# Kernel tuning notes

Measured on AMD Instinct MI355X. Metric: run time of the kernel, lower is better.

## Reference

```python
import jax, jax.numpy as jnp
import numpy as np

N = 50          # n_nodes
TAU = 1.0       # sinkhorn_tau
ITERS = 5       # sinkhorn_iters
ALPHA = 1.0


def _psi_fn(x, W1, b1, W2, b2):
    # x: [B, N, F]
    h = jax.nn.leaky_relu(x @ W1 + b1)          # [B, N, H], slope 0.01 matches torch default
    M = jax.nn.leaky_relu(h @ W2 + b2)          # [B, N, N]
    P = jnp.exp(M / TAU)
    for _ in range(ITERS):                      # alternating row/col normalization
        P = P / jnp.sum(P, axis=2, keepdims=True)
        P = P / jnp.sum(P, axis=1, keepdims=True)
    return P


def _hungarian(cost):
    """O(n^3) Hungarian (shortest augmenting path, like scipy.linear_sum_assignment).
    cost: [n, n] numpy. Returns col index assigned to each row (minimizes cost)."""
    n = cost.shape[0]
    INF = 1e18
    u = np.zeros(n + 1)
    v = np.zeros(n + 1)
    p = np.zeros(n + 1, dtype=np.int64)   # p[j] = row matched to column j (1-based)
    for i in range(1, n + 1):
        p[0] = i
        j0 = 0
        minv = np.full(n + 1, INF)
        way = np.zeros(n + 1, dtype=np.int64)
        used = np.zeros(n + 1, dtype=bool)
        while True:
            used[j0] = True
            i0 = p[j0]
            cur = cost[i0 - 1, :] - u[i0] - v[1:]
            free = ~used[1:]
            better = free & (cur < minv[1:])
            mv = minv[1:]
            mv[better] = cur[better]
            way[1:][better] = j0
            cand = np.where(free, mv, INF)
            j1 = int(np.argmin(cand)) + 1
            delta = cand[j1 - 1]
            u[p[used]] += delta
            v[used] -= delta
            mv[free] -= delta
            j0 = j1
            if p[j0] == 0:
                break
        while j0 != 0:
            j1 = way[j0]
            p[j0] = p[j1]
            j0 = j1
    row_to_col = np.zeros(n, dtype=np.int64)
    for j in range(1, n + 1):
        if p[j] > 0:
            row_to_col[p[j] - 1] = j - 1
    return row_to_col


def setup_inputs() -> dict:
    key = jax.random.key(0)
    k1, k2, k3, k4, k5 = jax.random.split(key, 5)
    B, F, H = 128, 1024, 4096
    s1 = 1.0 / np.sqrt(F)
    s2 = 1.0 / np.sqrt(H)
    x = jax.random.normal(k1, (B, N, F), dtype=jnp.float32)
    W1 = jax.random.uniform(k2, (F, H), minval=-s1, maxval=s1, dtype=jnp.float32)
    b1 = jax.random.uniform(k3, (H,), minval=-s1, maxval=s1, dtype=jnp.float32)
    W2 = jax.random.uniform(k4, (H, N), minval=-s2, maxval=s2, dtype=jnp.float32)
    b2 = jax.random.uniform(k5, (N,), minval=-s2, maxval=s2, dtype=jnp.float32)
    return {"x": x, "W1": W1, "b1": b1, "W2": W2, "b2": b2, "do_round": 1}


def reference(x, W1, b1, W2, b2, do_round):
    psi = _psi_fn(x, W1, b1, W2, b2)            # [B, N, N] doubly-stochastic (approx)
    if do_round:
        batch = np.asarray(psi)
        B = batch.shape[0]
        perms_np = np.zeros((B, N, N), dtype=np.float32)
        rows = np.arange(N)
        for i in range(B):
            cols = _hungarian(-batch[i])        # maximize psi == minimize -psi
            perms_np[i, rows, cols] = 1.0
        perms = jnp.asarray(perms_np)
        dist = jnp.sum(psi * perms, axis=(1, 2)) / N   # [B]
        X = (1.0 - ALPHA) * perms + ALPHA * psi
        return (psi, perms, X, dist)
    return (psi, None, None, None)
```

## Files before the change

### kernel.cpp

```cpp
#include <hip/hip_runtime.h>

#define NMAT 50
#define BATCH 128
#define FDIM 1024
#define HDIM 4096
#define ROWS 6400
#define PSIZE 320000
#define HINF 1e18

#define WS_M_OFF   0
#define WS_XH_OFF  10240000LL
#define WS_XL_OFF  23347200LL
#define WS_W1H_OFF 36454400LL
#define WS_W1L_OFF 44843008LL
#define WS_H_OFF   53231616LL
#define WS_MIN     (WS_H_OFF + 128LL * HDIM * 4)

typedef __bf16 bf16x8 __attribute__((ext_vector_type(8)));
typedef float f32x4 __attribute__((ext_vector_type(4)));
typedef double f64x4 __attribute__((ext_vector_type(4)));
typedef unsigned short u16;

__device__ __forceinline__ float bf16_to_f32(unsigned short h) {
  return __uint_as_float(((unsigned int)h) << 16);
}
__device__ __forceinline__ unsigned short f32_to_bf16(float f) {
  unsigned int u = __float_as_uint(f);
  u += 0x7FFFu + ((u >> 16) & 1u);
  return (unsigned short)(u >> 16);
}

__device__ __forceinline__ void gload16(const u16* g, u16* l) {
  __builtin_amdgcn_global_load_lds(
      (const __attribute__((address_space(1))) unsigned int*)g,
      (__attribute__((address_space(3))) unsigned int*)l, 16, 0, 0);
}

__device__ __forceinline__ double wave_min_f64(double x) {
  union { double d; int i[2]; } u, t;
  u.d = x;
#define DPP_MIN_STEP(ctrl)                                                   \
  t.i[0] = __builtin_amdgcn_update_dpp(u.i[0], u.i[0], ctrl, 0xf, 0xf, false);\
  t.i[1] = __builtin_amdgcn_update_dpp(u.i[1], u.i[1], ctrl, 0xf, 0xf, false);\
  u.d = fmin(u.d, t.d);
  DPP_MIN_STEP(0x111)
  DPP_MIN_STEP(0x112)
  DPP_MIN_STEP(0x114)
  DPP_MIN_STEP(0x118)
  DPP_MIN_STEP(0x142)
  DPP_MIN_STEP(0x143)
#undef DPP_MIN_STEP
  union { double d; int i[2]; } r;
  r.i[0] = __builtin_amdgcn_readlane(u.i[0], 63);
  r.i[1] = __builtin_amdgcn_readlane(u.i[1], 63);
  return r.d;
}

__global__ __launch_bounds__(256) void convert_x(
    const float* __restrict__ X, u16* __restrict__ Xh, u16* __restrict__ Xl) {
  int t = threadIdx.x;
  int mt = blockIdx.x >> 5, k0b = blockIdx.x & 31;
  size_t outbase = (size_t)blockIdx.x * 4096;
#pragma unroll
  for (int it = 0; it < 2; ++it) {
    int idx = t + it * 256;
    int m = idx & 127, kg = idx >> 7;
    const float* src = X + (size_t)(mt * 128 + m) * FDIM + k0b * 32 + kg * 8;
    float4 v0 = *(const float4*)src;
    float4 v1 = *(const float4*)(src + 4);
    float f[8] = {v0.x, v0.y, v0.z, v0.w, v1.x, v1.y, v1.z, v1.w};
    unsigned short h[8], l[8];
#pragma unroll
    for (int j = 0; j < 8; ++j) {
      h[j] = f32_to_bf16(f[j]);
      l[j] = f32_to_bf16(f[j] - bf16_to_f32(h[j]));
    }
    uint4 hv, lv;
    hv.x = h[0] | ((unsigned)h[1] << 16); hv.y = h[2] | ((unsigned)h[3] << 16);
    hv.z = h[4] | ((unsigned)h[5] << 16); hv.w = h[6] | ((unsigned)h[7] << 16);
    lv.x = l[0] | ((unsigned)l[1] << 16); lv.y = l[2] | ((unsigned)l[3] << 16);
    lv.z = l[4] | ((unsigned)l[5] << 16); lv.w = l[6] | ((unsigned)l[7] << 16);
    size_t off = outbase + (size_t)(kg * 128 + m) * 8;
    *(uint4*)&Xh[off] = hv;
    *(uint4*)&Xl[off] = lv;
  }
}

__global__ __launch_bounds__(256) void convert_w1(
    const float* __restrict__ W1, u16* __restrict__ Wh, u16* __restrict__ Wl) {
  int t = threadIdx.x;
  int nt = blockIdx.x >> 5, k0b = blockIdx.x & 31;
  size_t outbase = (size_t)blockIdx.x * 4096;
#pragma unroll
  for (int it = 0; it < 2; ++it) {
    int idx = t + it * 256;
    int n = idx & 127, kg = idx >> 7;
    float f[8];
#pragma unroll
    for (int j = 0; j < 8; ++j)
      f[j] = W1[(size_t)(k0b * 32 + kg * 8 + j) * HDIM + nt * 128 + n];
    unsigned short h[8], l[8];
#pragma unroll
    for (int j = 0; j < 8; ++j) {
      h[j] = f32_to_bf16(f[j]);
      l[j] = f32_to_bf16(f[j] - bf16_to_f32(h[j]));
    }
    uint4 hv, lv;
    hv.x = h[0] | ((unsigned)h[1] << 16); hv.y = h[2] | ((unsigned)h[3] << 16);
    hv.z = h[4] | ((unsigned)h[5] << 16); hv.w = h[6] | ((unsigned)h[7] << 16);
    lv.x = l[0] | ((unsigned)l[1] << 16); lv.y = l[2] | ((unsigned)l[3] << 16);
    lv.z = l[4] | ((unsigned)l[5] << 16); lv.w = l[6] | ((unsigned)l[7] << 16);
    size_t off = outbase + (size_t)(kg * 128 + n) * 8;
    *(uint4*)&Wh[off] = hv;
    *(uint4*)&Wl[off] = lv;
  }
}

__global__ __launch_bounds__(256) void gemm1_mfma(
    const u16* __restrict__ Ah_, const u16* __restrict__ Al_,
    const u16* __restrict__ Bh_, const u16* __restrict__ Bl_,
    const float* __restrict__ b1,
    float* __restrict__ Hout,
    int mt0) {
  __shared__ __align__(16) u16 Ah[4096];
  __shared__ __align__(16) u16 Al[4096];
  __shared__ __align__(16) u16 Bh[4096];
  __shared__ __align__(16) u16 Bl[4096];
  int t = threadIdx.x;
  int wave = t >> 6, lane = t & 63;
  int nt = blockIdx.x & 31;
  int mtl = blockIdx.x >> 5;
  int wm = wave >> 1, wn = wave & 1;
  int fr = lane & 15, fg = lane >> 4;

  f32x4 acc[4][4];
#pragma unroll
  for (int i = 0; i < 4; ++i)
#pragma unroll
    for (int j = 0; j < 4; ++j) acc[i][j] = (f32x4){0.f, 0.f, 0.f, 0.f};

  const u16* pAh = Ah_ + (size_t)(mt0 + mtl) * 32 * 4096;
  const u16* pAl = Al_ + (size_t)(mt0 + mtl) * 32 * 4096;
  const u16* pBh = Bh_ + (size_t)nt * 32 * 4096;
  const u16* pBl = Bl_ + (size_t)nt * 32 * 4096;
  int so = wave * 1024 + lane * 8;
  int ld = wave * 1024;

  for (int k0b = 0; k0b < 32; ++k0b) {
    __syncthreads();
    size_t sb = (size_t)k0b * 4096;
    gload16(pAh + sb + so,       &Ah[ld]);
    gload16(pAh + sb + so + 512, &Ah[ld + 512]);
    gload16(pAl + sb + so,       &Al[ld]);
    gload16(pAl + sb + so + 512, &Al[ld + 512]);
    gload16(pBh + sb + so,       &Bh[ld]);
    gload16(pBh + sb + so + 512, &Bh[ld + 512]);
    gload16(pBl + sb + so,       &Bl[ld]);
    gload16(pBl + sb + so + 512, &Bl[ld + 512]);
    __syncthreads();
    bf16x8 ah[4], al[4], bh[4], bl[4];
#pragma unroll
    for (int i = 0; i < 4; ++i) {
      int arow = (fg * 128 + wm * 64 + i * 16 + fr) * 8;
      ah[i] = *(const bf16x8*)&Ah[arow];
      al[i] = *(const bf16x8*)&Al[arow];
      int brow = (fg * 128 + wn * 64 + i * 16 + fr) * 8;
      bh[i] = *(const bf16x8*)&Bh[brow];
      bl[i] = *(const bf16x8*)&Bl[brow];
    }
#pragma unroll
    for (int i = 0; i < 4; ++i)
#pragma unroll
      for (int j = 0; j < 4; ++j)
        acc[i][j] = __builtin_amdgcn_mfma_f32_16x16x32_bf16(ah[i], bh[j], acc[i][j], 0, 0, 0);
#pragma unroll
    for (int i = 0; i < 4; ++i)
#pragma unroll
      for (int j = 0; j < 4; ++j)
        acc[i][j] = __builtin_amdgcn_mfma_f32_16x16x32_bf16(ah[i], bl[j], acc[i][j], 0, 0, 0);
#pragma unroll
    for (int i = 0; i < 4; ++i)
#pragma unroll
      for (int j = 0; j < 4; ++j)
        acc[i][j] = __builtin_amdgcn_mfma_f32_16x16x32_bf16(al[i], bh[j], acc[i][j], 0, 0, 0);
  }

  int colb = nt * 128 + wn * 64 + fr;
  int rowb = mtl * 128 + wm * 64 + fg * 4;
#pragma unroll
  for (int j = 0; j < 4; ++j) {
    float bias = b1[colb + j * 16];
#pragma unroll
    for (int i = 0; i < 4; ++i)
#pragma unroll
      for (int r = 0; r < 4; ++r) {
        float v = acc[i][j][r] + bias;
        v = v >= 0.0f ? v : 0.01f * v;
        Hout[(size_t)(rowb + i * 16 + r) * HDIM + colb + j * 16] = v;
      }
  }
}

__global__ __launch_bounds__(256) void gemm2_mfma(
    const float* __restrict__ hchunk,
    const float* __restrict__ W2,
    double* __restrict__ Mpart,
    int row0) {
  __shared__ __align__(16) float hs[64 * 68];
  __shared__ __align__(16) float w2s[64 * 68];
  int t = threadIdx.x;
  int wave = t >> 6, lane = t & 63;
  int kz = blockIdx.y;
  int fr = lane & 15, fk = lane >> 4;
  const float* hbase = hchunk + (size_t)blockIdx.x * 64 * HDIM;

  f64x4 z4 = (f64x4){0.0, 0.0, 0.0, 0.0};
  f64x4 pA = __builtin_amdgcn_mfma_f64_16x16x4f64((double)lane, 1.0, z4, 0, 0, 0);
  f64x4 pB = __builtin_amdgcn_mfma_f64_16x16x4f64(1.0, (double)lane, z4, 0, 0, 0);
  int aAlt = ((int)pA[0]) & 3;
  int bAlt = ((int)pB[0]) & 3;
  int ai = aAlt ? (lane >> 2) : fr;
  int ak = aAlt ? (lane & 3) : fk;
  int bj = bAlt ? (lane >> 2) : fr;
  int bk = bAlt ? (lane & 3) : fk;
  f64x4 p1 = __builtin_amdgcn_mfma_f64_16x16x4f64((double)ai, 1.0, z4, 0, 0, 0);
  f64x4 p2 = __builtin_amdgcn_mfma_f64_16x16x4f64(1.0, (double)bj, z4, 0, 0, 0);
  int di[4], dj[4];
#pragma unroll
  for (int r = 0; r < 4; ++r) {
    di[r] = (((int)p1[r]) >> 2) & 15;
    dj[r] = (((int)p2[r]) >> 2) & 15;
  }

  f64x4 acc[4], acc2[4];
#pragma unroll
  for (int nt = 0; nt < 4; ++nt) { acc[nt] = z4; acc2[nt] = z4; }

  int arow = (wave * 16 + ai) * 68 + ak;
  for (int k0 = kz * 1024; k0 < kz * 1024 + 1024; k0 += 64) {
    __syncthreads();
    {
      int row = t >> 2, seg = (t & 3) * 16;
      const float4* src = (const float4*)(hbase + (size_t)row * HDIM + k0 + seg);
      float4* dst = (float4*)&hs[row * 68 + seg];
      dst[0] = src[0]; dst[1] = src[1]; dst[2] = src[2]; dst[3] = src[3];
    }
    for (int idx = t; idx < 64 * 64; idx += 256) {
      int kk = idx >> 6, n = idx & 63;
      w2s[kk * 68 + n] = (n < NMAT) ? W2[(size_t)(k0 + kk) * NMAT + n] : 0.0f;
    }
    __syncthreads();
#pragma unroll
    for (int kk = 0; kk < 64; kk += 8) {
      double av0 = (double)hs[arow + kk];
      double av1 = (double)hs[arow + kk + 4];
#pragma unroll
      for (int nt = 0; nt < 4; ++nt) {
        double bv = (double)w2s[(kk + bk) * 68 + nt * 16 + bj];
        acc[nt] = __builtin_amdgcn_mfma_f64_16x16x4f64(av0, bv, acc[nt], 0, 0, 0);
      }
#pragma unroll
      for (int nt = 0; nt < 4; ++nt) {
        double bv = (double)w2s[(kk + 4 + bk) * 68 + nt * 16 + bj];
        acc2[nt] = __builtin_amdgcn_mfma_f64_16x16x4f64(av1, bv, acc2[nt], 0, 0, 0);
      }
    }
  }
  double* Mout = Mpart + (size_t)kz * PSIZE;
  int rowbase = row0 + blockIdx.x * 64 + wave * 16;
#pragma unroll
  for (int nt = 0; nt < 4; ++nt) {
    f64x4 s = acc[nt] + acc2[nt];
#pragma unroll
    for (int r = 0; r < 4; ++r) {
      int col = nt * 16 + dj[r];
      if (col < NMAT)
        Mout[(size_t)(rowbase + di[r]) * NMAT + col] = s[r];
    }
  }
}

__global__ __launch_bounds__(64) void sinkhorn_hungarian(
    const double* __restrict__ Mpart, const float* __restrict__ b2,
    float* __restrict__ out_psi, float* __restrict__ out_X,
    float* __restrict__ out_perms, float* __restrict__ out_dist) {
  int b = blockIdx.x, lane = threadIdx.x;
  __shared__ double P[2500];
  __shared__ double cost[2500];
  __shared__ double rs[50];
  __shared__ double u[51];
  __shared__ int p[51];
  __shared__ int wayl[51];
  const size_t base = (size_t)b * 2500;

  for (int e = lane; e < 2500; e += 64) {
    double m = Mpart[base + e] + Mpart[PSIZE + base + e] +
               Mpart[2 * PSIZE + base + e] + Mpart[3 * PSIZE + base + e];
    m += (double)b2[e % 50];
    m = m >= 0.0 ? m : 0.01 * m;
    P[e] = exp(m);
  }
  __syncthreads();
  for (int it = 0; it < 5; ++it) {
    if (lane < 50) { double s = 0; for (int j = 0; j < 50; ++j) s += P[lane * 50 + j]; rs[lane] = s; }
    __syncthreads();
    for (int e = lane; e < 2500; e += 64) P[e] /= rs[e / 50];
    __syncthreads();
    if (lane < 50) { double s = 0; for (int r = 0; r < 50; ++r) s += P[r * 50 + lane]; rs[lane] = s; }
    __syncthreads();
    for (int e = lane; e < 2500; e += 64) P[e] /= rs[e % 50];
    __syncthreads();
  }
  for (int e = lane; e < 2500; e += 64) {
    float f = (float)P[e];
    out_psi[base + e] = f;
    out_X[base + e] = f;
    cost[e] = -P[e];
  }
  if (lane < 51) { u[lane] = 0.0; p[lane] = 0; }
  __syncthreads();

  double v = 0.0;
  bool lactive = lane < NMAT;
  for (int i = 1; i <= NMAT; ++i) {
    bool used = false;
    int way = 0;
    int j0 = 0, j1 = 0;
    for (int guard = 0; guard < 64; ++guard) {
      if (lane == j0 - 1) used = true;
      int i0 = (j0 == 0) ? i : p[j0];
      double ui0 = u[i0];
      double cand = HINF;
      if (lactive && !used) {
        cand = cost[(i0 - 1) * NMAT + lane] - ui0 - v;
        way = j0;
      }
      double m = wave_min_f64(cand);
      unsigned long long bal = __ballot(cand == m);
      j1 = (int)__builtin_ctzll(bal) + 1;
      double delta = m;
      __syncthreads();
      if (used) { v -= delta; u[p[lane + 1]] += delta; }
      if (lane == 63) u[i] += delta;
      __syncthreads();
      j0 = j1;
      if (p[j0] == 0) break;
    }
    if (lactive) wayl[lane + 1] = way;
    __syncthreads();
    if (lane == 0) {
      int j = j1;
      for (int step = 0; step < 64 && j != 0; ++step) {
        int jw = wayl[j];
        p[j] = (jw == 0) ? i : p[jw];
        j = jw;
      }
    }
    __syncthreads();
  }

  size_t pbase = (size_t)b * 2500;
  for (int e = lane; e < 2500; e += 64) out_perms[pbase + e] = 0.0f;
  __syncthreads();
  double val = 0.0;
  if (lactive) {
    int row = p[lane + 1] - 1;
    if (row < 0) row = 0;
    if (row > 49) row = 49;
    out_perms[pbase + (size_t)row * NMAT + lane] = 1.0f;
    val = P[(size_t)row * NMAT + lane];
  }
#pragma unroll
  for (int s = 32; s > 0; s >>= 1) val += __shfl_xor(val, s, 64);
  if (lane == 0) out_dist[b] = (float)(val / (double)NMAT);
}

extern "C" void kernel_launch(void* const* d_in, const int* in_sizes, int n_in,
                              void* d_out, int out_size, void* d_ws, size_t ws_size,
                              hipStream_t stream) {
  const float* x  = (const float*)d_in[0];
  const float* W1 = (const float*)d_in[1];
  const float* b1 = (const float*)d_in[2];
  const float* W2 = (const float*)d_in[3];
  const float* b2 = (const float*)d_in[4];
  float* out = (float*)d_out;
  float* out_psi   = out;
  float* out_perms = out + PSIZE;
  float* out_X     = out + 2 * PSIZE;
  float* out_dist  = out + 3 * PSIZE;

  if (ws_size < (size_t)WS_MIN) return;

  char* ws = (char*)d_ws;
  double* Mpart = (double*)(ws + WS_M_OFF);
  u16* Xh  = (u16*)(ws + WS_XH_OFF);
  u16* Xl  = (u16*)(ws + WS_XL_OFF);
  u16* W1h = (u16*)(ws + WS_W1H_OFF);
  u16* W1l = (u16*)(ws + WS_W1L_OFF);
  float* hbuf = (float*)(ws + WS_H_OFF);
  long long avail = (long long)ws_size - WS_H_OFF;
  int max_rows = (int)(avail / (HDIM * 4));
  max_rows = (max_rows / 128) * 128;
  if (max_rows > ROWS) max_rows = ROWS;

  hipLaunchKernelGGL(convert_x, dim3(1600), dim3(256), 0, stream, x, Xh, Xl);
  hipLaunchKernelGGL(convert_w1, dim3(1024), dim3(256), 0, stream, W1, W1h, W1l);

  for (int r0 = 0; r0 < ROWS; r0 += max_rows) {
    int rows = (ROWS - r0 < max_rows) ? (ROWS - r0) : max_rows;
    hipLaunchKernelGGL(gemm1_mfma, dim3((rows / 128) * 32), dim3(256), 0, stream,
                       Xh, Xl, W1h, W1l, b1, hbuf, r0 / 128);
    hipLaunchKernelGGL(gemm2_mfma, dim3(rows / 64, 4), dim3(256), 0, stream,
                       hbuf, W2, Mpart, r0);
  }
  hipLaunchKernelGGL(sinkhorn_hungarian, dim3(BATCH), dim3(64), 0, stream,
                     Mpart, b2, out_psi, out_X, out_perms, out_dist);
}
```

Before: 554.5 us.

## Transpose hidden buffer and restructure fp64 second GEMM with wider K-split

gemm1 now writes the hidden activations transposed (column-major by hidden unit) using float4 stores. gemm2 becomes a single-wave kernel that reads directly from global memory without LDS staging, uses a zero-padded W2 prepared by a new conversion kernel, and splits K into 8 partitions instead of 4. The aim is more parallel blocks and less shared-memory and synchronisation overhead in the fp64 GEMM, paid for by a larger partial-sum buffer, more partial reductions in the sinkhorn kernel, and strided global reads with no reuse across waves.

```diff
diff --git a/kernel.cpp b/kernel.cpp
--- a/kernel.cpp
+++ b/kernel.cpp
@@ -6,14 +6,16 @@
 #define HDIM 4096
 #define ROWS 6400
 #define PSIZE 320000
+#define NPART 8
 #define HINF 1e18
 
 #define WS_M_OFF   0
-#define WS_XH_OFF  10240000LL
-#define WS_XL_OFF  23347200LL
-#define WS_W1H_OFF 36454400LL
-#define WS_W1L_OFF 44843008LL
-#define WS_H_OFF   53231616LL
+#define WS_XH_OFF  20480000LL
+#define WS_XL_OFF  33587200LL
+#define WS_W1H_OFF 46694400LL
+#define WS_W1L_OFF 55083008LL
+#define WS_W2P_OFF 63471616LL
+#define WS_H_OFF   64520192LL
 #define WS_MIN     (WS_H_OFF + 128LL * HDIM * 4)
 
 typedef __bf16 bf16x8 __attribute__((ext_vector_type(8)));
@@ -116,12 +118,19 @@
   }
 }
 
+__global__ __launch_bounds__(256) void convert_w2(
+    const float* __restrict__ W2, float* __restrict__ W2p) {
+  int idx = blockIdx.x * 256 + threadIdx.x;
+  int k = idx >> 6, n = idx & 63;
+  W2p[idx] = (n < NMAT) ? W2[(size_t)k * NMAT + n] : 0.0f;
+}
+
 __global__ __launch_bounds__(256) void gemm1_mfma(
     const u16* __restrict__ Ah_, const u16* __restrict__ Al_,
     const u16* __restrict__ Bh_, const u16* __restrict__ Bl_,
     const float* __restrict__ b1,
-    float* __restrict__ Hout,
-    int mt0) {
+    float* __restrict__ HTout,
+    int mt0, int stride) {
   __shared__ __align__(16) u16 Ah[4096];
   __shared__ __align__(16) u16 Al[4096];
   __shared__ __align__(16) u16 Bh[4096];
@@ -191,28 +200,27 @@
   for (int j = 0; j < 4; ++j) {
     float bias = b1[colb + j * 16];
 #pragma unroll
-    for (int i = 0; i < 4; ++i)
+    for (int i = 0; i < 4; ++i) {
+      float4 v4;
+      float* vp = &v4.x;
 #pragma unroll
       for (int r = 0; r < 4; ++r) {
         float v = acc[i][j][r] + bias;
-        v = v >= 0.0f ? v : 0.01f * v;
-        Hout[(size_t)(rowb + i * 16 + r) * HDIM + colb + j * 16] = v;
+        vp[r] = v >= 0.0f ? v : 0.01f * v;
       }
-  }
-}
-
-__global__ __launch_bounds__(256) void gemm2_mfma(
-    const float* __restrict__ hchunk,
-    const float* __restrict__ W2,
+      *(float4*)&HTout[(size_t)(colb + j * 16) * stride + rowb + i * 16] = v4;
+    }
+  }
+}
+
+__global__ __launch_bounds__(64) void gemm2_mfma(
+    const float* __restrict__ hT,
+    const float* __restrict__ W2p,
     double* __restrict__ Mpart,
-    int row0) {
-  __shared__ __align__(16) float hs[64 * 68];
-  __shared__ __align__(16) float w2s[64 * 68];
-  int t = threadIdx.x;
-  int wave = t >> 6, lane = t & 63;
+    int row0, int stride) {
+  int lane = threadIdx.x;
   int kz = blockIdx.y;
   int fr = lane & 15, fk = lane >> 4;
-  const float* hbase = hchunk + (size_t)blockIdx.x * 64 * HDIM;
 
   f64x4 z4 = (f64x4){0.0, 0.0, 0.0, 0.0};
   f64x4 pA = __builtin_amdgcn_mfma_f64_16x16x4f64((double)lane, 1.0, z4, 0, 0, 0);
@@ -232,52 +240,32 @@
     dj[r] = (((int)p2[r]) >> 2) & 15;
   }
 
-  f64x4 acc[4], acc2[4];
-#pragma unroll
-  for (int nt = 0; nt < 4; ++nt) { acc[nt] = z4; acc2[nt] = z4; }
-
-  int arow = (wave * 16 + ai) * 68 + ak;
-  for (int k0 = kz * 1024; k0 < kz * 1024 + 1024; k0 += 64) {
-    __syncthreads();
-    {
-      int row = t >> 2, seg = (t & 3) * 16;
-      const float4* src = (const float4*)(hbase + (size_t)row * HDIM + k0 + seg);
-      float4* dst = (float4*)&hs[row * 68 + seg];
-      dst[0] = src[0]; dst[1] = src[1]; dst[2] = src[2]; dst[3] = src[3];
-    }
-    for (int idx = t; idx < 64 * 64; idx += 256) {
-      int kk = idx >> 6, n = idx & 63;
-      w2s[kk * 68 + n] = (n < NMAT) ? W2[(size_t)(k0 + kk) * NMAT + n] : 0.0f;
-    }
-    __syncthreads();
-#pragma unroll
-    for (int kk = 0; kk < 64; kk += 8) {
-      double av0 = (double)hs[arow + kk];
-      double av1 = (double)hs[arow + kk + 4];
-#pragma unroll
-      for (int nt = 0; nt < 4; ++nt) {
-        double bv = (double)w2s[(kk + bk) * 68 + nt * 16 + bj];
-        acc[nt] = __builtin_amdgcn_mfma_f64_16x16x4f64(av0, bv, acc[nt], 0, 0, 0);
-      }
-#pragma unroll
-      for (int nt = 0; nt < 4; ++nt) {
-        double bv = (double)w2s[(kk + 4 + bk) * 68 + nt * 16 + bj];
-        acc2[nt] = __builtin_amdgcn_mfma_f64_16x16x4f64(av1, bv, acc2[nt], 0, 0, 0);
-      }
-    }
-  }
+  f64x4 acc[4];
+#pragma unroll
+  for (int nt = 0; nt < 4; ++nt) acc[nt] = z4;
+
+  const float* hA = hT + blockIdx.x * 16 + ai;
+  const int kend = kz * (FDIM * 4 / NPART) + (FDIM * 4 / NPART);
+#pragma unroll 4
+  for (int k = kz * (FDIM * 4 / NPART); k < kend; k += 4) {
+    double av = (double)hA[(size_t)(k + ak) * stride];
+#pragma unroll
+    for (int nt = 0; nt < 4; ++nt) {
+      double bv = (double)W2p[(k + bk) * 64 + nt * 16 + bj];
+      acc[nt] = __builtin_amdgcn_mfma_f64_16x16x4f64(av, bv, acc[nt], 0, 0, 0);
+    }
+  }
+
   double* Mout = Mpart + (size_t)kz * PSIZE;
-  int rowbase = row0 + blockIdx.x * 64 + wave * 16;
-#pragma unroll
-  for (int nt = 0; nt < 4; ++nt) {
-    f64x4 s = acc[nt] + acc2[nt];
+  int rowbase = row0 + blockIdx.x * 16;
+#pragma unroll
+  for (int nt = 0; nt < 4; ++nt)
 #pragma unroll
     for (int r = 0; r < 4; ++r) {
       int col = nt * 16 + dj[r];
       if (col < NMAT)
-        Mout[(size_t)(rowbase + di[r]) * NMAT + col] = s[r];
-    }
-  }
+        Mout[(size_t)(rowbase + di[r]) * NMAT + col] = acc[nt][r];
+    }
 }
 
 __global__ __launch_bounds__(64) void sinkhorn_hungarian(
@@ -294,8 +282,10 @@
   const size_t base = (size_t)b * 2500;
 
   for (int e = lane; e < 2500; e += 64) {
-    double m = Mpart[base + e] + Mpart[PSIZE + base + e] +
-               Mpart[2 * PSIZE + base + e] + Mpart[3 * PSIZE + base + e];
+    double m = 0.0;
+#pragma unroll
+    for (int pz = 0; pz < NPART; ++pz)
+      m += Mpart[(size_t)pz * PSIZE + base + e];
     m += (double)b2[e % 50];
     m = m >= 0.0 ? m : 0.01 * m;
     P[e] = exp(m);
@@ -397,6 +387,7 @@
   u16* Xl  = (u16*)(ws + WS_XL_OFF);
   u16* W1h = (u16*)(ws + WS_W1H_OFF);
   u16* W1l = (u16*)(ws + WS_W1L_OFF);
+  float* W2p  = (float*)(ws + WS_W2P_OFF);
   float* hbuf = (float*)(ws + WS_H_OFF);
   long long avail = (long long)ws_size - WS_H_OFF;
   int max_rows = (int)(avail / (HDIM * 4));
@@ -405,13 +396,14 @@
 
   hipLaunchKernelGGL(convert_x, dim3(1600), dim3(256), 0, stream, x, Xh, Xl);
   hipLaunchKernelGGL(convert_w1, dim3(1024), dim3(256), 0, stream, W1, W1h, W1l);
+  hipLaunchKernelGGL(convert_w2, dim3(1024), dim3(256), 0, stream, W2, W2p);
 
   for (int r0 = 0; r0 < ROWS; r0 += max_rows) {
     int rows = (ROWS - r0 < max_rows) ? (ROWS - r0) : max_rows;
     hipLaunchKernelGGL(gemm1_mfma, dim3((rows / 128) * 32), dim3(256), 0, stream,
-                       Xh, Xl, W1h, W1l, b1, hbuf, r0 / 128);
-    hipLaunchKernelGGL(gemm2_mfma, dim3(rows / 64, 4), dim3(256), 0, stream,
-                       hbuf, W2, Mpart, r0);
+                       Xh, Xl, W1h, W1l, b1, hbuf, r0 / 128, rows);
+    hipLaunchKernelGGL(gemm2_mfma, dim3(rows / 16, NPART), dim3(64), 0, stream,
+                       hbuf, W2p, Mpart, r0, rows);
   }
   hipLaunchKernelGGL(sinkhorn_hungarian, dim3(BATCH), dim3(64), 0, stream,
                      Mpart, b2, out_psi, out_X, out_perms, out_dist);
```

New measurement: 561.2 us. About the same (+1.2%).
